# Kernel tuning notes

Hardware: AMD Instinct MI355X
Metric: run time of the kernel (lower is better)

The kernel has to match this reference:

```python
import jax, jax.numpy as jnp
import numpy as np

MIN_BIN_WIDTH = 1e-3
MIN_BIN_HEIGHT = 1e-3
MIN_DERIVATIVE = 1e-3
TAIL_BOUND = 1.0
N_POS = 2097152
N_CHANNELS = 8
N_BINS = 128
DEFAULT_INIT = float(np.log(np.exp(1.0 - MIN_DERIVATIVE) - 1.0))


def setup_inputs() -> dict:
    key = jax.random.key(0)
    k1, k2, k3, k4 = jax.random.split(key, 4)
    # positions rescaled to roughly [-1, 1]; include slight tail overshoot
    x = jax.random.uniform(k1, (N_POS, N_CHANNELS), minval=-1.1, maxval=1.1, dtype=jnp.float32)
    uw = DEFAULT_INIT + 0.1 * jax.random.normal(k2, (N_CHANNELS, N_BINS), dtype=jnp.float32)
    uh = DEFAULT_INIT + 0.1 * jax.random.normal(k3, (N_CHANNELS, N_BINS), dtype=jnp.float32)
    ud = DEFAULT_INIT + 0.1 * jax.random.normal(k4, (N_CHANNELS, N_BINS - 1), dtype=jnp.float32)
    return {"x": x, "unnormalized_widths": uw, "unnormalized_heights": uh,
            "unnormalized_derivatives": ud}


def _bin_edges(unnormalized, min_size, left, right):
    # softmax-normalized sizes with a minimum bin size, cumsum -> knot locations
    n_bins = unnormalized.shape[-1]
    sizes = jax.nn.softmax(unnormalized, axis=-1)
    sizes = min_size + (1.0 - min_size * n_bins) * sizes
    cum = jnp.cumsum(sizes, axis=-1)
    cum = jnp.pad(cum, ((0, 0), (1, 0)))
    cum = (right - left) * cum + left
    cum = cum.at[..., 0].set(left).at[..., -1].set(right)
    sizes = cum[..., 1:] - cum[..., :-1]
    return sizes, cum


def _log_prob(x, uw, uh, ud):
    left, right = -TAIL_BOUND, TAIL_BOUND
    bottom, top = -TAIL_BOUND, TAIL_BOUND
    C = uw.shape[0]

    widths, cumwidths = _bin_edges(uw * 10.0, MIN_BIN_WIDTH, left, right)      # (C,B),(C,B+1)
    heights, cumheights = _bin_edges(uh * 10.0, MIN_BIN_HEIGHT, bottom, top)   # (C,B),(C,B+1)
    ud_pad = jnp.pad(ud, ((0, 0), (1, 1)), constant_values=DEFAULT_INIT)       # linear tails
    derivatives = MIN_DERIVATIVE + jax.nn.softplus(ud_pad)                      # (C,B+1)
    delta = heights / widths                                                    # (C,B)

    inside = (x >= left) & (x <= right)
    xc = jnp.clip(x, bottom, top)  # inverse pass searches over cumheights

    edges = cumheights.at[:, -1].add(1e-6)
    # per-channel bin search, memory-light searchsorted
    idx = jax.vmap(lambda e, v: jnp.searchsorted(e, v, side='right'),
                   in_axes=(0, 1), out_axes=1)(edges, xc) - 1                   # (N,C)
    idx = jnp.clip(idx, 0, widths.shape[-1] - 1)

    ch = jnp.arange(C)[None, :]
    icw = cumwidths[ch, idx]
    ibw = widths[ch, idx]
    ich = cumheights[ch, idx]
    ih = heights[ch, idx]
    idl = delta[ch, idx]
    d0 = derivatives[ch, idx]
    d1 = derivatives[ch, idx + 1]

    # quadratic inverse solve (Durkan et al. rational-quadratic spline)
    dy = xc - ich
    t = d0 + d1 - 2.0 * idl
    a = dy * t + ih * (idl - d0)
    b = ih * d0 - dy * t
    c = -idl * dy
    disc = jnp.maximum(b * b - 4.0 * a * c, 0.0)
    root = (2.0 * c) / (-b - jnp.sqrt(disc))
    theta_1m = root * (1.0 - root)
    denom = idl + t * theta_1m
    der_num = (idl ** 2) * (d1 * root ** 2 + 2.0 * idl * theta_1m + d0 * (1.0 - root) ** 2)
    logabsdet = jnp.log(der_num) - 2.0 * jnp.log(denom)
    logdet = jnp.where(inside, -logabsdet, 0.0)  # identity tails -> logdet 0
    return np.log(0.5).astype(np.float32) + logdet


def reference(x, unnormalized_widths, unnormalized_heights, unnormalized_derivatives):
    return _log_prob(x, unnormalized_widths, unnormalized_heights, unnormalized_derivatives)
```

## Files before the change

kernel.cpp:

```cpp
#include <hip/hip_runtime.h>
#include <math.h>


#define NB 128
#define NCH 8
#define NSLOT 1024
#define E_F 0
#define P4_F 1032
#define HINT_F 5160
#define TAB_FLOATS 7208

typedef float v2f __attribute__((ext_vector_type(2)));

__global__ __launch_bounds__(128) void spline_precompute(
    const float* __restrict__ uw, const float* __restrict__ uh,
    const float* __restrict__ ud, float* __restrict__ ws)
{
    const int c = blockIdx.x;
    const int i = threadIdx.x;
    __shared__ float red[128];
    __shared__ float scan[128];
    __shared__ float cum[129];
    __shared__ float wdt[128];
    __shared__ float sdv[129];
    const float DEFAULT_INIT = logf(expf(1.0f - 1e-3f) - 1.0f);

    float v = uw[c * NB + i] * 10.0f;
    red[i] = v; __syncthreads();
    #pragma unroll
    for (int s = 64; s >= 1; s >>= 1) { if (i < s) red[i] = fmaxf(red[i], red[i + s]); __syncthreads(); }
    float ex = expf(v - red[0]);
    __syncthreads();
    red[i] = ex; __syncthreads();
    #pragma unroll
    for (int s = 64; s >= 1; s >>= 1) { if (i < s) red[i] += red[i + s]; __syncthreads(); }
    float sz = 1e-3f + (1.0f - 1e-3f * NB) * (ex / red[0]);
    __syncthreads();
    scan[i] = sz;
    for (int off = 1; off < NB; off <<= 1) {
        __syncthreads();
        float t = (i >= off) ? scan[i - off] : 0.0f;
        __syncthreads();
        scan[i] += t;
    }
    __syncthreads();
    if (i == 0) cum[0] = -1.0f;
    cum[i + 1] = (i == NB - 1) ? 1.0f : fmaf(2.0f, scan[i], -1.0f);
    __syncthreads();
    wdt[i] = cum[i + 1] - cum[i];
    __syncthreads();

    v = uh[c * NB + i] * 10.0f;
    red[i] = v; __syncthreads();
    #pragma unroll
    for (int s = 64; s >= 1; s >>= 1) { if (i < s) red[i] = fmaxf(red[i], red[i + s]); __syncthreads(); }
    ex = expf(v - red[0]);
    __syncthreads();
    red[i] = ex; __syncthreads();
    #pragma unroll
    for (int s = 64; s >= 1; s >>= 1) { if (i < s) red[i] += red[i + s]; __syncthreads(); }
    sz = 1e-3f + (1.0f - 1e-3f * NB) * (ex / red[0]);
    __syncthreads();
    scan[i] = sz;
    for (int off = 1; off < NB; off <<= 1) {
        __syncthreads();
        float t = (i >= off) ? scan[i - off] : 0.0f;
        __syncthreads();
        scan[i] += t;
    }
    __syncthreads();
    if (i == 0) cum[0] = -1.0f;
    cum[i + 1] = (i == NB - 1) ? 1.0f : fmaf(2.0f, scan[i], -1.0f);

    float u0 = (i == 0) ? DEFAULT_INIT : ud[c * (NB - 1) + i - 1];
    sdv[i] = 1e-3f + log1pf(expf(u0));
    if (i == NB - 1) sdv[NB] = 1e-3f + log1pf(expf(DEFAULT_INIT));
    __syncthreads();

    float hh  = cum[i + 1] - cum[i];
    float idl = hh / wdt[i];
    const int o = c * 129 + i;

    ws[E_F + o] = cum[i];
    if (i == NB - 1) ws[E_F + c * 129 + NB] = 1.0f + 1e-6f;
    float4* g_p4 = reinterpret_cast<float4*>(ws + P4_F);
    g_p4[o] = make_float4(hh, idl, sdv[i], sdv[i + 1]);

    unsigned char* g_hint = reinterpret_cast<unsigned char*>(ws + HINT_F);
    for (int s = i; s < NSLOT; s += NB) {
        float left = (float)s * (2.0f / NSLOT) - 1.0f;
        int k = 0;
        #pragma unroll
        for (int st = 64; st >= 1; st >>= 1) {
            int t = k + st;
            if (cum[t] <= left) k = t;
        }
        g_hint[c * NSLOT + s] = (unsigned char)k;
    }
}

__global__ __launch_bounds__(256, 4) void spline_main(
    const float4* __restrict__ x4, float4* __restrict__ out4,
    const float* __restrict__ ws, int npair)
{
    __shared__ __align__(16) float tab[TAB_FLOATS];
    {
        float4* dst = reinterpret_cast<float4*>(tab);
        const float4* src = reinterpret_cast<const float4*>(ws);
        for (int t = threadIdx.x; t < TAB_FLOATS / 4; t += 256) dst[t] = src[t];
    }
    __syncthreads();
    const float* eg = tab + E_F;
    const float4* p4 = reinterpret_cast<const float4*>(tab + P4_F);
    const unsigned char* hint = reinterpret_cast<const unsigned char*>(tab + HINT_F);

    const float LOG_HALF = -0.6931471805599453f;
    const float LN2 = 0.6931471805599453f;
    const int tid = blockIdx.x * 256 + threadIdx.x;
    const int stride = gridDim.x * 256;

    float4 pfa, pfb;
    if (tid < npair) { pfa = x4[2 * tid]; pfb = x4[2 * tid + 1]; }

    for (int i = tid; i < npair; i += stride) {
        float4 xa = pfa, xb = pfb;
        int inx = i + stride;
        inx = (inx < npair) ? inx : i;
        pfa = x4[2 * inx];
        pfb = x4[2 * inx + 1];

        float xs[8] = {xa.x, xa.y, xa.z, xa.w, xb.x, xb.y, xb.z, xb.w};

        float xq[8];
        int kk[8];
        #pragma unroll
        for (int j = 0; j < 8; ++j) {
            float xc = fminf(fmaxf(xs[j], -1.0f), 1.0f);
            xq[j] = xc;
            int s = (int)fmaf(xc, (float)(NSLOT / 2), (float)(NSLOT / 2));
            s = (s > NSLOT - 1) ? NSLOT - 1 : s;
            kk[j] = hint[j * NSLOT + s];
        }

        float e0[8], e1[8];
        #pragma unroll
        for (int j = 0; j < 8; ++j) {
            const float* ej = eg + j * 129 + kk[j];
            e0[j] = ej[0];
            e1[j] = ej[1];
        }

        float4 pk[8];
        float dyv[8], lm[8];
        #pragma unroll
        for (int j = 0; j < 8; ++j) {
            bool adv = (e1[j] <= xq[j]);
            int k2 = kk[j] + (adv ? 1 : 0);
            float ich = adv ? e1[j] : e0[j];
            dyv[j] = xq[j] - ich;
            lm[j] = (xs[j] == xq[j]) ? LN2 : 0.0f;
            pk[j] = p4[j * 129 + k2];
        }

        float rs[8];
        #pragma unroll
        for (int jj = 0; jj < 4; ++jj) {
            v2f h  = {pk[jj].x, pk[jj + 4].x};
            v2f dl = {pk[jj].y, pk[jj + 4].y};
            v2f d0 = {pk[jj].z, pk[jj + 4].z};
            v2f d1 = {pk[jj].w, pk[jj + 4].w};
            v2f dy = {dyv[jj],  dyv[jj + 4]};
            const v2f m2 = {-2.0f, -2.0f};
            const v2f m4 = {-4.0f, -4.0f};
            const v2f zz = {0.0f, 0.0f};

            v2f T    = __builtin_elementwise_fma(m2, dl, d0 + d1);
            v2f dyt  = dy * T;
            v2f B    = h * d0;
            v2f A    = __builtin_elementwise_fma(h, dl, -B);
            v2f aa   = dyt + A;
            v2f bb   = B - dyt;
            v2f cc   = -dl * dy;
            v2f ac   = aa * cc;
            v2f disc = __builtin_elementwise_max(
                           __builtin_elementwise_fma(m4, ac, bb * bb), zz);
            v2f sq   = {__builtin_amdgcn_sqrtf(disc.x),
                        __builtin_amdgcn_sqrtf(disc.y)};
            v2f w    = -bb - sq;
            v2f u    = cc + cc;
            v2f w2   = w * w;
            v2f tu   = T * u;
            v2f sdd  = dl - d0;
            v2f E    = sdd + sdd;
            v2f t1   = __builtin_elementwise_fma(E, w, tu);
            v2f num  = __builtin_elementwise_fma(t1, u, d0 * w2);
            v2f d2   = dl * dl;
            v2f numf = (num * w2) * d2;
            v2f wmu  = w - u;
            v2f denb = __builtin_elementwise_fma(tu, wmu, dl * w2);
            v2f den2 = denb * denb;

            float va = __fdividef(numf.x, den2.x);
            float vb = __fdividef(numf.y, den2.y);
            rs[jj]     = fmaf(-lm[jj],     __log2f(va), LOG_HALF);
            rs[jj + 4] = fmaf(-lm[jj + 4], __log2f(vb), LOG_HALF);
        }

        out4[2 * i]     = make_float4(rs[0], rs[1], rs[2], rs[3]);
        out4[2 * i + 1] = make_float4(rs[4], rs[5], rs[6], rs[7]);
    }
}

extern "C" void kernel_launch(void* const* d_in, const int* in_sizes, int n_in,
                              void* d_out, int out_size, void* d_ws, size_t ws_size,
                              hipStream_t stream) {
    const float* x  = (const float*)d_in[0];
    const float* uw = (const float*)d_in[1];
    const float* uh = (const float*)d_in[2];
    const float* ud = (const float*)d_in[3];
    float* ws = (float*)d_ws;

    spline_precompute<<<NCH, NB, 0, stream>>>(uw, uh, ud, ws);

    const int npair = out_size / 8;
    spline_main<<<1280, 256, 0, stream>>>(
        (const float4*)x, (float4*)d_out, ws, npair);
}
```

Before: 42.42 us.

## Software-pipeline LDS table gathers against spline math in half-row groups

Splits each 8-channel row into two 4-channel groups and interleaves the table gathers for one group with the quadratic solve and store of the other, prefetching x two groups ahead. The aim is to hide LDS gather latency behind ALU work within a thread. The grid shrinks to 1024 blocks, and the loop count is computed as npair/stride, which drops any remainder rows when npair is not a multiple of the stride.

```diff
diff --git a/kernel.cpp b/kernel.cpp
--- a/kernel.cpp
+++ b/kernel.cpp
@@ -118,58 +118,51 @@
     const float LN2 = 0.6931471805599453f;
     const int tid = blockIdx.x * 256 + threadIdx.x;
     const int stride = gridDim.x * 256;
-
-    float4 pfa, pfb;
-    if (tid < npair) { pfa = x4[2 * tid]; pfb = x4[2 * tid + 1]; }
-
-    for (int i = tid; i < npair; i += stride) {
-        float4 xa = pfa, xb = pfb;
-        int inx = i + stride;
-        inx = (inx < npair) ? inx : i;
-        pfa = x4[2 * inx];
-        pfb = x4[2 * inx + 1];
-
-        float xs[8] = {xa.x, xa.y, xa.z, xa.w, xb.x, xb.y, xb.z, xb.w};
-
-        float xq[8];
-        int kk[8];
-        #pragma unroll
-        for (int j = 0; j < 8; ++j) {
+    const int niter = npair / stride;
+    const int ng = 2 * niter;
+
+    auto idx4 = [&](int g) {
+        int gg = (g < ng) ? g : 0;
+        return 2 * (tid + (gg >> 1) * stride) + (gg & 1);
+    };
+
+    auto gather4 = [&](const float4& xv, int CB, float4* pk, float* dy, float* lmf) {
+        float xs[4] = {xv.x, xv.y, xv.z, xv.w};
+        float xq[4]; int kk[4];
+        #pragma unroll
+        for (int j = 0; j < 4; ++j) {
             float xc = fminf(fmaxf(xs[j], -1.0f), 1.0f);
             xq[j] = xc;
             int s = (int)fmaf(xc, (float)(NSLOT / 2), (float)(NSLOT / 2));
             s = (s > NSLOT - 1) ? NSLOT - 1 : s;
-            kk[j] = hint[j * NSLOT + s];
-        }
-
-        float e0[8], e1[8];
-        #pragma unroll
-        for (int j = 0; j < 8; ++j) {
-            const float* ej = eg + j * 129 + kk[j];
+            kk[j] = hint[(CB + j) * NSLOT + s];
+        }
+        float e0[4], e1[4];
+        #pragma unroll
+        for (int j = 0; j < 4; ++j) {
+            const float* ej = eg + (CB + j) * 129 + kk[j];
             e0[j] = ej[0];
             e1[j] = ej[1];
         }
-
-        float4 pk[8];
-        float dyv[8], lm[8];
-        #pragma unroll
-        for (int j = 0; j < 8; ++j) {
+        #pragma unroll
+        for (int j = 0; j < 4; ++j) {
             bool adv = (e1[j] <= xq[j]);
             int k2 = kk[j] + (adv ? 1 : 0);
-            float ich = adv ? e1[j] : e0[j];
-            dyv[j] = xq[j] - ich;
-            lm[j] = (xs[j] == xq[j]) ? LN2 : 0.0f;
-            pk[j] = p4[j * 129 + k2];
-        }
-
-        float rs[8];
-        #pragma unroll
-        for (int jj = 0; jj < 4; ++jj) {
-            v2f h  = {pk[jj].x, pk[jj + 4].x};
-            v2f dl = {pk[jj].y, pk[jj + 4].y};
-            v2f d0 = {pk[jj].z, pk[jj + 4].z};
-            v2f d1 = {pk[jj].w, pk[jj + 4].w};
-            v2f dy = {dyv[jj],  dyv[jj + 4]};
+            dy[j]  = xq[j] - (adv ? e1[j] : e0[j]);
+            lmf[j] = (xs[j] == xq[j]) ? LN2 : 0.0f;
+            pk[j]  = p4[(CB + j) * 129 + k2];
+        }
+    };
+
+    auto mathstore = [&](const float4* pk, const float* dy4, const float* lmf, int oidx) {
+        float rs[4];
+        #pragma unroll
+        for (int jj = 0; jj < 2; ++jj) {
+            v2f h  = {pk[jj].x, pk[jj + 2].x};
+            v2f dl = {pk[jj].y, pk[jj + 2].y};
+            v2f d0 = {pk[jj].z, pk[jj + 2].z};
+            v2f d1 = {pk[jj].w, pk[jj + 2].w};
+            v2f dy = {dy4[jj],  dy4[jj + 2]};
             const v2f m2 = {-2.0f, -2.0f};
             const v2f m4 = {-4.0f, -4.0f};
             const v2f zz = {0.0f, 0.0f};
@@ -202,12 +195,28 @@
 
             float va = __fdividef(numf.x, den2.x);
             float vb = __fdividef(numf.y, den2.y);
-            rs[jj]     = fmaf(-lm[jj],     __log2f(va), LOG_HALF);
-            rs[jj + 4] = fmaf(-lm[jj + 4], __log2f(vb), LOG_HALF);
-        }
-
-        out4[2 * i]     = make_float4(rs[0], rs[1], rs[2], rs[3]);
-        out4[2 * i + 1] = make_float4(rs[4], rs[5], rs[6], rs[7]);
+            rs[jj]     = fmaf(-lmf[jj],     __log2f(va), LOG_HALF);
+            rs[jj + 2] = fmaf(-lmf[jj + 2], __log2f(vb), LOG_HALF);
+        }
+        out4[oidx] = make_float4(rs[0], rs[1], rs[2], rs[3]);
+    };
+
+    float4 pkA[4], pkB[4];
+    float dyA[4], dyB[4], lmA[4], lmB[4];
+
+    float4 xg0 = x4[idx4(0)];
+    float4 xg1 = x4[idx4(1)];
+    gather4(xg0, 0, pkA, dyA, lmA);
+    float4 xg2 = x4[idx4(2)];
+
+    #pragma unroll 1
+    for (int g = 0; g < ng; g += 2) {
+        gather4(xg1, 4, pkB, dyB, lmB);
+        xg1 = x4[idx4(g + 3)];
+        mathstore(pkA, dyA, lmA, idx4(g));
+        gather4(xg2, 0, pkA, dyA, lmA);
+        xg2 = x4[idx4(g + 4)];
+        mathstore(pkB, dyB, lmB, idx4(g + 1));
     }
 }
 
@@ -223,6 +232,6 @@
     spline_precompute<<<NCH, NB, 0, stream>>>(uw, uh, ud, ws);
 
     const int npair = out_size / 8;
-    spline_main<<<1280, 256, 0, stream>>>(
+    spline_main<<<1024, 256, 0, stream>>>(
         (const float4*)x, (float4*)d_out, ws, npair);
 }
```

New measurement: 42.47 us. About the same (+0.1%).

## Pack per-bin params as fp16, shrink LDS table, raise occupancy and grid

Applied to the files above, without the earlier changes.

Stores per-bin delta, d0 and the precomputed T as fp16 in an 8-byte record instead of a float4, and derives bin height from adjacent edge loads. This shrinks the shared table so more blocks fit per CU, and launch bounds and grid size are raised to match. The hint table gains a slot so the clamp is dropped, and the input clamp uses med3. fp16 params lose precision in the log-det, which may hurt accuracy.

```diff
diff --git a/kernel.cpp b/kernel.cpp
--- a/kernel.cpp
+++ b/kernel.cpp
@@ -5,12 +5,18 @@
 #define NB 128
 #define NCH 8
 #define NSLOT 1024
-#define E_F 0
-#define P4_F 1032
-#define HINT_F 5160
-#define TAB_FLOATS 7208
+#define PACK_B 4128
+#define HINT_B 12384
+#define TAB_FLOATS 5148
 
 typedef float v2f __attribute__((ext_vector_type(2)));
+typedef _Float16 h4 __attribute__((ext_vector_type(4)));
+
+static __device__ inline unsigned short f2h(float v) {
+    union { _Float16 h; unsigned short u; } c;
+    c.h = (_Float16)v;
+    return c.u;
+}
 
 __global__ __launch_bounds__(128) void spline_precompute(
     const float* __restrict__ uw, const float* __restrict__ uh,
@@ -79,15 +85,20 @@
 
     float hh  = cum[i + 1] - cum[i];
     float idl = hh / wdt[i];
+    float d0v = sdv[i], d1v = sdv[i + 1];
+    float Tv  = d0v + d1v - 2.0f * idl;
     const int o = c * 129 + i;
 
-    ws[E_F + o] = cum[i];
-    if (i == NB - 1) ws[E_F + c * 129 + NB] = 1.0f + 1e-6f;
-    float4* g_p4 = reinterpret_cast<float4*>(ws + P4_F);
-    g_p4[o] = make_float4(hh, idl, sdv[i], sdv[i + 1]);
-
-    unsigned char* g_hint = reinterpret_cast<unsigned char*>(ws + HINT_F);
-    for (int s = i; s < NSLOT; s += NB) {
+    ws[o] = cum[i];
+    if (i == NB - 1) ws[c * 129 + NB] = 1.0f + 1e-6f;
+
+    ushort4* g_pk = reinterpret_cast<ushort4*>(reinterpret_cast<char*>(ws) + PACK_B);
+    g_pk[o] = make_ushort4(f2h(idl), f2h(d0v), f2h(Tv), 0);
+    if (i == NB - 1)
+        g_pk[o + 1] = make_ushort4(f2h(1.0f), f2h(1.0f), 0, 0);
+
+    unsigned char* g_hint = reinterpret_cast<unsigned char*>(ws) + HINT_B;
+    for (int s = i; s < NSLOT + 1; s += NB) {
         float left = (float)s * (2.0f / NSLOT) - 1.0f;
         int k = 0;
         #pragma unroll
@@ -95,11 +106,11 @@
             int t = k + st;
             if (cum[t] <= left) k = t;
         }
-        g_hint[c * NSLOT + s] = (unsigned char)k;
-    }
-}
-
-__global__ __launch_bounds__(256, 4) void spline_main(
+        g_hint[c * (NSLOT + 1) + s] = (unsigned char)k;
+    }
+}
+
+__global__ __launch_bounds__(256, 6) void spline_main(
     const float4* __restrict__ x4, float4* __restrict__ out4,
     const float* __restrict__ ws, int npair)
 {
@@ -110,9 +121,9 @@
         for (int t = threadIdx.x; t < TAB_FLOATS / 4; t += 256) dst[t] = src[t];
     }
     __syncthreads();
-    const float* eg = tab + E_F;
-    const float4* p4 = reinterpret_cast<const float4*>(tab + P4_F);
-    const unsigned char* hint = reinterpret_cast<const unsigned char*>(tab + HINT_F);
+    const float* eg = tab;
+    const h4* ph = reinterpret_cast<const h4*>(reinterpret_cast<const char*>(tab) + PACK_B);
+    const unsigned char* hint = reinterpret_cast<const unsigned char*>(tab) + HINT_B;
 
     const float LOG_HALF = -0.6931471805599453f;
     const float LN2 = 0.6931471805599453f;
@@ -135,51 +146,51 @@
         int kk[8];
         #pragma unroll
         for (int j = 0; j < 8; ++j) {
-            float xc = fminf(fmaxf(xs[j], -1.0f), 1.0f);
+            float xc = __builtin_amdgcn_fmed3f(xs[j], -1.0f, 1.0f);
             xq[j] = xc;
             int s = (int)fmaf(xc, (float)(NSLOT / 2), (float)(NSLOT / 2));
-            s = (s > NSLOT - 1) ? NSLOT - 1 : s;
-            kk[j] = hint[j * NSLOT + s];
-        }
-
-        float e0[8], e1[8];
+            kk[j] = hint[j * (NSLOT + 1) + s];
+        }
+
+        float e0[8], e1[8], e2[8];
         #pragma unroll
         for (int j = 0; j < 8; ++j) {
             const float* ej = eg + j * 129 + kk[j];
             e0[j] = ej[0];
             e1[j] = ej[1];
-        }
-
-        float4 pk[8];
-        float dyv[8], lm[8];
+            e2[j] = ej[2];
+        }
+
+        h4 hv[8];
+        float dyv[8], hb[8], lm[8];
         #pragma unroll
         for (int j = 0; j < 8; ++j) {
             bool adv = (e1[j] <= xq[j]);
             int k2 = kk[j] + (adv ? 1 : 0);
-            float ich = adv ? e1[j] : e0[j];
-            dyv[j] = xq[j] - ich;
+            float elo = adv ? e1[j] : e0[j];
+            float ehi = adv ? e2[j] : e1[j];
+            dyv[j] = xq[j] - elo;
+            hb[j]  = ehi - elo;
             lm[j] = (xs[j] == xq[j]) ? LN2 : 0.0f;
-            pk[j] = p4[j * 129 + k2];
+            hv[j] = ph[j * 129 + k2];
         }
 
         float rs[8];
         #pragma unroll
         for (int jj = 0; jj < 4; ++jj) {
-            v2f h  = {pk[jj].x, pk[jj + 4].x};
-            v2f dl = {pk[jj].y, pk[jj + 4].y};
-            v2f d0 = {pk[jj].z, pk[jj + 4].z};
-            v2f d1 = {pk[jj].w, pk[jj + 4].w};
-            v2f dy = {dyv[jj],  dyv[jj + 4]};
-            const v2f m2 = {-2.0f, -2.0f};
+            v2f dl = {(float)hv[jj].x, (float)hv[jj + 4].x};
+            v2f d0 = {(float)hv[jj].y, (float)hv[jj + 4].y};
+            v2f T  = {(float)hv[jj].z, (float)hv[jj + 4].z};
+            v2f h  = {hb[jj],  hb[jj + 4]};
+            v2f dy = {dyv[jj], dyv[jj + 4]};
             const v2f m4 = {-4.0f, -4.0f};
             const v2f zz = {0.0f, 0.0f};
 
-            v2f T    = __builtin_elementwise_fma(m2, dl, d0 + d1);
             v2f dyt  = dy * T;
-            v2f B    = h * d0;
-            v2f A    = __builtin_elementwise_fma(h, dl, -B);
-            v2f aa   = dyt + A;
-            v2f bb   = B - dyt;
+            v2f sdd  = dl - d0;
+            v2f E    = sdd + sdd;
+            v2f aa   = __builtin_elementwise_fma(h, sdd, dyt);
+            v2f bb   = __builtin_elementwise_fma(h, d0, -dyt);
             v2f cc   = -dl * dy;
             v2f ac   = aa * cc;
             v2f disc = __builtin_elementwise_max(
@@ -190,8 +201,6 @@
             v2f u    = cc + cc;
             v2f w2   = w * w;
             v2f tu   = T * u;
-            v2f sdd  = dl - d0;
-            v2f E    = sdd + sdd;
             v2f t1   = __builtin_elementwise_fma(E, w, tu);
             v2f num  = __builtin_elementwise_fma(t1, u, d0 * w2);
             v2f d2   = dl * dl;
@@ -223,6 +232,6 @@
     spline_precompute<<<NCH, NB, 0, stream>>>(uw, uh, ud, ws);
 
     const int npair = out_size / 8;
-    spline_main<<<1280, 256, 0, stream>>>(
+    spline_main<<<1792, 256, 0, stream>>>(
         (const float4*)x, (float4*)d_out, ws, npair);
 }
```

Result: faster. 41.57 us (-2.0%).
